# Kernel optimization log

Measured on AMD Instinct MI355X. Metric: run time of the kernel, lower is better.

## Reference

```python
import jax, jax.numpy as jnp
import numpy as np

EMBED_DIM = 512
NUM_HEADS = 8
HEAD_DIM = EMBED_DIM // NUM_HEADS
GRID = 48
BATCH = 8


def _locality_bias(grid_h, grid_w):
    # normalised negative squared L2 distances between patch centres, in [-1, 0]
    gy, gx = jnp.meshgrid(jnp.linspace(0.0, 1.0, grid_h),
                          jnp.linspace(0.0, 1.0, grid_w), indexing='ij')
    coords = jnp.stack([gy.reshape(-1), gx.reshape(-1)], axis=-1)  # (N, 2)
    diff = coords[None, :, :] - coords[:, None, :]                 # (N, N, 2)
    dist2 = jnp.sum(diff * diff, axis=-1)                          # (N, N)
    return -dist2 / jnp.max(dist2)


def setup_inputs() -> dict:
    key = jax.random.key(0)
    k_x, k_qkv, k_pw, k_pb, k_t, k_lw = jax.random.split(key, 6)
    N = GRID * GRID
    x = jax.random.normal(k_x, (BATCH, N, EMBED_DIM), dtype=jnp.float32)
    # torch nn.Linear weights are (out_features, in_features)
    qkv_w = jax.random.normal(k_qkv, (3 * EMBED_DIM, EMBED_DIM), dtype=jnp.float32) * 0.02
    proj_w = jax.random.normal(k_pw, (EMBED_DIM, EMBED_DIM), dtype=jnp.float32) * 0.02
    proj_b = jax.random.normal(k_pb, (EMBED_DIM,), dtype=jnp.float32) * 0.02
    init_temp = float(np.log(HEAD_DIM ** (-0.5)))
    temperature = init_temp + 0.02 * jax.random.normal(k_t, (NUM_HEADS, 1, 1), dtype=jnp.float32)
    locality_weight = 0.1 + 0.02 * jax.random.normal(k_lw, (NUM_HEADS,), dtype=jnp.float32)
    return {
        'x': x,
        'qkv_w': qkv_w,
        'proj_w': proj_w,
        'proj_b': proj_b,
        'temperature': temperature,
        'locality_weight': locality_weight,
        'grid_h': GRID,
        'grid_w': GRID,
    }


def reference(x, qkv_w, proj_w, proj_b, temperature, locality_weight, grid_h, grid_w):
    B, N, C = x.shape
    H = temperature.shape[0]
    D = C // H
    # qkv projection (no bias): (B, N, 3C) -> (3, B, H, N, D)
    qkv = (x @ qkv_w.T).reshape(B, N, 3, H, D)
    qkv = jnp.transpose(qkv, (2, 0, 3, 1, 4))
    q, k, v = qkv[0], qkv[1], qkv[2]              # each (B, H, N, D)
    scale = jnp.exp(temperature)                  # (H, 1, 1) learnable per-head temp
    attn = jnp.einsum('bhqd,bhkd->bhqk', q, k) * scale[None]
    loc = _locality_bias(grid_h, grid_w)          # (N, N), values in [-1, 0]
    attn = attn + locality_weight[None, :, None, None] * loc[None, None]
    attn = jax.nn.softmax(attn, axis=-1)          # dropout is identity (p=0 / eval)
    out = jnp.einsum('bhqk,bhkd->bhqd', attn, v)  # (B, H, N, D)
    out = jnp.transpose(out, (0, 2, 1, 3)).reshape(B, N, C)
    return out @ proj_w.T + proj_b
```

## Files before the change

### kernel.cpp

```cpp
#include <hip/hip_runtime.h>

typedef unsigned int   uint_ma   __attribute__((may_alias));
typedef unsigned short ushort_ma __attribute__((may_alias));
typedef float          float_ma  __attribute__((may_alias));
typedef __bf16 bf16x8 __attribute__((ext_vector_type(8)));
typedef float f32x4 __attribute__((ext_vector_type(4)));
typedef uint_ma u32x4 __attribute__((ext_vector_type(4)));
typedef ushort_ma u16x4 __attribute__((ext_vector_type(4)));

#define BATCH 8
#define NTOK 2304
#define CDIM 512
#define NH 8
#define HD 64
#define MROWS (BATCH * NTOK)
#define LOG2E 1.44269504088896f

constexpr size_t N_X  = (size_t)BATCH * NTOK * CDIM;
constexpr size_t N_WQ = (size_t)3 * CDIM * CDIM;
constexpr size_t N_WP = (size_t)CDIM * CDIM;
constexpr size_t OFF_XO = 0;
constexpr size_t OFF_WQ = OFF_XO + N_X;
constexpr size_t OFF_WP = OFF_WQ + N_WQ;
constexpr size_t OFF_Q  = OFF_WP + N_WP;
constexpr size_t OFF_K  = OFF_Q + N_X;
constexpr size_t OFF_V  = OFF_K + N_X;
constexpr size_t CV8 = (N_X + N_WQ + N_WP) / 8;

__device__ __forceinline__ float bf2f(unsigned short h) {
  unsigned int u = ((unsigned int)h) << 16;
  return __builtin_bit_cast(float, u);
}
__device__ __forceinline__ unsigned short f2bf(float f) {
  unsigned int u = __builtin_bit_cast(unsigned int, f);
  u += 0x7fffu + ((u >> 16) & 1u);
  return (unsigned short)(u >> 16);
}

__device__ __forceinline__ void gload16(const void* g, void* l) {
  __builtin_amdgcn_global_load_lds(
      (const __attribute__((address_space(1))) void*)g,
      (__attribute__((address_space(3))) void*)l, 16, 0, 0);
}

__global__ __launch_bounds__(256) void convert3(
    const float* __restrict__ s0, const float* __restrict__ s1,
    const float* __restrict__ s2, ushort_ma* __restrict__ base) {
  const size_t gid = (size_t)blockIdx.x * blockDim.x + threadIdx.x;
  const size_t stride = (size_t)gridDim.x * blockDim.x;
  for (size_t i = gid; i < CV8; i += stride) {
    size_t r = i;
    const float* src;
    size_t doff;
    if (r < N_X / 8) { src = s0; doff = OFF_XO; }
    else if ((r -= N_X / 8) < N_WQ / 8) { src = s1; doff = OFF_WQ; }
    else { r -= N_WQ / 8; src = s2; doff = OFF_WP; }
    const f32x4* fw = (const f32x4*)(src + r * 8);
    const f32x4 a = fw[0], b = fw[1];
    u16x4 lo, hi;
#pragma unroll
    for (int j = 0; j < 4; j++) { lo[j] = f2bf(a[j]); hi[j] = f2bf(b[j]); }
    ushort_ma* dst = base + doff + r * 8;
    *(u16x4*)dst = lo;
    *(u16x4*)(dst + 4) = hi;
  }
}

template <int MODE>
__global__ __launch_bounds__(256, 3) void gemm_bt(
    const ushort_ma* __restrict__ A, const ushort_ma* __restrict__ W,
    const float* __restrict__ aux,
    unsigned short* __restrict__ o0,
    unsigned short* __restrict__ o1,
    unsigned short* __restrict__ o2)
{
  __shared__ __align__(16) ushort_ma As[2][128][32];
  __shared__ __align__(16) ushort_ma Bs[2][128][32];
  const int K = CDIM;
  const int m0 = blockIdx.x * 128;
  const int n0 = blockIdx.y * 128;
  const int t = threadIdx.x;
  const int lane = t & 63;
  const int w = t >> 6;
  const int wm = (w >> 1) * 64, wn = (w & 1) * 64;
  const int lr = lane & 15, lq = lane >> 4;

  const int srow = w * 16 + (lane >> 2);
  const int scg = (lane & 3) ^ ((srow >> 1) & 3);
  const ushort_ma* Ag0 = A + (size_t)(m0 + srow) * K + scg * 8;
  const ushort_ma* Ag1 = Ag0 + (size_t)64 * K;
  const ushort_ma* Bg0 = W + (size_t)(n0 + srow) * K + scg * 8;
  const ushort_ma* Bg1 = Bg0 + (size_t)64 * K;

  const f32x4 fz = {0.f, 0.f, 0.f, 0.f};
  f32x4 acc[4][4];
#pragma unroll
  for (int i = 0; i < 4; i++)
#pragma unroll
    for (int j = 0; j < 4; j++) acc[i][j] = fz;

  auto issue = [&](int kt, int buf) {
    const int k0 = kt * 32;
    gload16(Ag0 + k0, (void*)&As[buf][w * 16][0]);
    gload16(Ag1 + k0, (void*)&As[buf][64 + w * 16][0]);
    gload16(Bg0 + k0, (void*)&Bs[buf][w * 16][0]);
    gload16(Bg1 + k0, (void*)&Bs[buf][64 + w * 16][0]);
  };

  issue(0, 0);
  const int colf = 8 * (lq ^ ((lr >> 1) & 3));

  for (int kt = 0; kt < 16; kt++) {
    const int buf = kt & 1;
    __syncthreads();
    if (kt < 15) issue(kt + 1, buf ^ 1);
    bf16x8 af[4], bfr[4];
#pragma unroll
    for (int i = 0; i < 4; i++)
      af[i] = __builtin_bit_cast(bf16x8, *(const u32x4*)(&As[buf][wm + i * 16 + lr][colf]));
#pragma unroll
    for (int j = 0; j < 4; j++)
      bfr[j] = __builtin_bit_cast(bf16x8, *(const u32x4*)(&Bs[buf][wn + j * 16 + lr][colf]));
#pragma unroll
    for (int i = 0; i < 4; i++)
#pragma unroll
      for (int j = 0; j < 4; j++)
        acc[i][j] = __builtin_amdgcn_mfma_f32_16x16x32_bf16(af[i], bfr[j], acc[i][j], 0, 0, 0);
  }

  if (MODE == 0) {
#pragma unroll
    for (int j = 0; j < 4; j++) {
      const int gc = n0 + wn + j * 16 + lr;
      const int which = gc >> 9;
      const int h = (gc >> 6) & 7;
      const int d = gc & 63;
#pragma unroll
      for (int i = 0; i < 4; i++) {
        const int gm0 = m0 + wm + i * 16 + lq * 4;
        const int b = gm0 / NTOK;
        const int np = gm0 - b * NTOK;
        if (which == 2) {
          u16x4 pk;
#pragma unroll
          for (int r = 0; r < 4; r++) pk[r] = f2bf(acc[i][j][r]);
          *(u16x4*)(o2 + ((size_t)((b * NH + h) * HD + d)) * NTOK + np) = pk;
        } else {
          const float sc = (which == 0) ? __expf(aux[h]) * LOG2E : 1.0f;
          unsigned short* dst = (which == 0) ? o0 : o1;
          const size_t base = ((size_t)((b * NH + h) * NTOK + np)) * HD + d;
#pragma unroll
          for (int r = 0; r < 4; r++) dst[base + (size_t)r * HD] = f2bf(acc[i][j][r] * sc);
        }
      }
    }
  } else {
    float_ma* outf = (float_ma*)o0;
#pragma unroll
    for (int j = 0; j < 4; j++) {
      const int gc = n0 + wn + j * 16 + lr;
      const float bv = aux[gc];
#pragma unroll
      for (int i = 0; i < 4; i++) {
        const int gm0 = m0 + wm + i * 16 + lq * 4;
#pragma unroll
        for (int r = 0; r < 4; r++)
          outf[(size_t)(gm0 + r) * CDIM + gc] = acc[i][j][r] + bv;
      }
    }
  }
}

__global__ __launch_bounds__(256, 3) void attn_kernel(
    const ushort_ma* __restrict__ Qg,
    const ushort_ma* __restrict__ Kg,
    const ushort_ma* __restrict__ Vg,
    const float* __restrict__ lwp,
    unsigned short* __restrict__ Og)
{
  __shared__ __align__(16) ushort_ma Ks[128][104];
  __shared__ __align__(16) ushort_ma Vs[64][136];
  __shared__ __align__(16) ushort_ma Ps[4][32][32];

  const int bh = blockIdx.y;
  const int b = bh >> 3, h = bh & 7;
  const int q0 = blockIdx.x * 128;
  const int t = threadIdx.x;
  const int lane = t & 63;
  const int w = t >> 6;
  const int lr = lane & 15, lq = lane >> 4;

  if (t < 128) {
    const u32x4 z4 = {0u, 0u, 0u, 0u};
    *(u32x4*)(&Ks[t][72]) = z4;
    *(u32x4*)(&Ks[t][80]) = z4;
    *(u32x4*)(&Ks[t][88]) = z4;
  }
  {
    const ushort_ma* Qb = Qg + ((size_t)bh * NTOK + q0) * HD;
#pragma unroll
    for (int it = 0; it < 4; it++) {
      const int q = t + it * 256;
      const int row = q >> 3, seg = (q & 7) * 8;
      *(u32x4*)(&Ks[row][seg]) = *(const u32x4*)(Qb + (size_t)row * HD + seg);
    }
  }
  __syncthreads();
  bf16x8 aQ[2][2];
#pragma unroll
  for (int mi = 0; mi < 2; mi++)
#pragma unroll
    for (int ks = 0; ks < 2; ks++)
      aQ[mi][ks] = __builtin_bit_cast(
          bf16x8, *(const u32x4*)(&Ks[w * 32 + mi * 16 + lr][ks * 32 + lq * 8]));

  const float cb2 = -0.5f * LOG2E * lwp[h];
  bf16x8 aQb[2];
#pragma unroll
  for (int mi = 0; mi < 2; mi++) {
    const int qrow = q0 + w * 32 + mi * 16 + lr;
    const int yy = qrow / 48;
    const int xx = qrow - yy * 48;
    const float fy = (float)yy * (1.0f / 47.0f);
    const float fx = (float)xx * (1.0f / 47.0f);
    u32x4 v = {0u, 0u, 0u, 0u};
    if (lq == 0) {
      v[0] = (unsigned int)f2bf(fy) | ((unsigned int)f2bf(fx) << 16);
      v[1] = (unsigned int)f2bf(fy * fy + fx * fx) | (0x3F80u << 16);
    }
    aQb[mi] = __builtin_bit_cast(bf16x8, v);
  }

  const u32x4 onesU = {0x3F803F80u, 0x3F803F80u, 0x3F803F80u, 0x3F803F80u};
  const bf16x8 bOnes = __builtin_bit_cast(bf16x8, onesU);

  const f32x4 fz = {0.f, 0.f, 0.f, 0.f};
  f32x4 accO[2][4];
  f32x4 accL[2];
#pragma unroll
  for (int mi = 0; mi < 2; mi++) {
    accL[mi] = fz;
#pragma unroll
    for (int nd = 0; nd < 4; nd++) accO[mi][nd] = fz;
  }

  const ushort_ma* Kb = Kg + (size_t)bh * NTOK * HD;
  const ushort_ma* Vb = Vg + (size_t)bh * HD * NTOK;

  for (int kt = 0; kt < 18; kt++) {
    const int kv0 = kt * 128;
    __syncthreads();
    u32x4 kc[4], vc[4];
#pragma unroll
    for (int it = 0; it < 4; it++) {
      const int q = t + it * 256;
      kc[it] = *(const u32x4*)(Kb + (size_t)(kv0 + (q >> 3)) * HD + (q & 7) * 8);
      vc[it] = *(const u32x4*)(Vb + (size_t)(q >> 4) * NTOK + kv0 + (q & 15) * 8);
    }
#pragma unroll
    for (int it = 0; it < 4; it++) {
      const int q = t + it * 256;
      *(u32x4*)(&Ks[q >> 3][(q & 7) * 8]) = kc[it];
      *(u32x4*)(&Vs[q >> 4][(q & 15) * 8]) = vc[it];
    }
    if (t < 128) {
      const int kv = kv0 + t;
      const int yy = kv / 48;
      const int xx = kv - yy * 48;
      const float fy = (float)yy * (1.0f / 47.0f);
      const float fx = (float)xx * (1.0f / 47.0f);
      u32x4 bv;
      bv[0] = (unsigned int)f2bf(-2.0f * cb2 * fy) |
              ((unsigned int)f2bf(-2.0f * cb2 * fx) << 16);
      bv[1] = (unsigned int)f2bf(cb2) |
              ((unsigned int)f2bf(cb2 * (fy * fy + fx * fx)) << 16);
      bv[2] = 0u;
      bv[3] = 0u;
      *(u32x4*)(&Ks[t][64]) = bv;
    }
    __syncthreads();

#pragma unroll
    for (int c = 0; c < 4; c++) {
      f32x4 s2[2][2] = {{fz, fz}, {fz, fz}};
#pragma unroll
      for (int e2 = 0; e2 < 2; e2++) {
        const int ni = 2 * c + e2;
#pragma unroll
        for (int ks = 0; ks < 3; ks++) {
          const bf16x8 bK = __builtin_bit_cast(
              bf16x8, *(const u32x4*)(&Ks[ni * 16 + lr][ks * 32 + lq * 8]));
#pragma unroll
          for (int mi = 0; mi < 2; mi++) {
            const bf16x8 aOp = (ks < 2) ? aQ[mi][ks] : aQb[mi];
            s2[mi][e2] = __builtin_amdgcn_mfma_f32_16x16x32_bf16(aOp, bK, s2[mi][e2], 0, 0, 0);
          }
        }
      }
#pragma unroll
      for (int e2 = 0; e2 < 2; e2++) {
#pragma unroll
        for (int mi = 0; mi < 2; mi++)
#pragma unroll
          for (int r = 0; r < 4; r++) {
            const float p = __builtin_amdgcn_exp2f(s2[mi][e2][r]);
            const unsigned int pu = __builtin_bit_cast(unsigned int, p);
            const int fw = (2 * lq + (r >> 1)) & 3;
            const int gcol = 8 * ((e2 * 2 + (lr >> 3)) ^ fw) + (lr & 7);
            Ps[w][mi * 16 + lq * 4 + r][gcol] = (unsigned short)(pu >> 16);
          }
      }
      __asm__ volatile("s_waitcnt lgkmcnt(0)" ::: "memory");
      bf16x8 aP[2];
#pragma unroll
      for (int mi = 0; mi < 2; mi++)
        aP[mi] = __builtin_bit_cast(
            bf16x8,
            *(const u32x4*)(&Ps[w][mi * 16 + lr][8 * (lq ^ ((lr >> 1) & 3))]));
#pragma unroll
      for (int nd = 0; nd < 4; nd++) {
        const bf16x8 bV = __builtin_bit_cast(
            bf16x8, *(const u32x4*)(&Vs[nd * 16 + lr][c * 32 + lq * 8]));
#pragma unroll
        for (int mi = 0; mi < 2; mi++)
          accO[mi][nd] = __builtin_amdgcn_mfma_f32_16x16x32_bf16(aP[mi], bV, accO[mi][nd], 0, 0, 0);
      }
#pragma unroll
      for (int mi = 0; mi < 2; mi++)
        accL[mi] = __builtin_amdgcn_mfma_f32_16x16x32_bf16(aP[mi], bOnes, accL[mi], 0, 0, 0);
    }
  }

#pragma unroll
  for (int mi = 0; mi < 2; mi++) {
    f32x4 inv;
#pragma unroll
    for (int r = 0; r < 4; r++) inv[r] = 1.0f / accL[mi][r];
#pragma unroll
    for (int nd = 0; nd < 4; nd++)
#pragma unroll
      for (int r = 0; r < 4; r++) {
        const int np = q0 + w * 32 + mi * 16 + lq * 4 + r;
        Og[((size_t)(b * NTOK + np)) * CDIM + h * HD + nd * 16 + lr] =
            f2bf(accO[mi][nd][r] * inv[r]);
      }
  }
}

extern "C" void kernel_launch(void* const* d_in, const int* in_sizes, int n_in,
                              void* d_out, int out_size, void* d_ws, size_t ws_size,
                              hipStream_t stream) {
  const float* x      = (const float*)d_in[0];
  const float* qkv_w  = (const float*)d_in[1];
  const float* proj_w = (const float*)d_in[2];
  const float* proj_b = (const float*)d_in[3];
  const float* temp   = (const float*)d_in[4];
  const float* lw     = (const float*)d_in[5];

  ushort_ma* base = (ushort_ma*)d_ws;
  ushort_ma* XB  = base + OFF_XO;
  ushort_ma* WQB = base + OFF_WQ;
  ushort_ma* WPB = base + OFF_WP;
  ushort_ma* Q   = base + OFF_Q;
  ushort_ma* Kt  = base + OFF_K;
  ushort_ma* Vt  = base + OFF_V;
  ushort_ma* O   = XB;

  convert3<<<1024, 256, 0, stream>>>(x, qkv_w, proj_w, base);
  gemm_bt<0><<<dim3(MROWS / 128, 1536 / 128), 256, 0, stream>>>(
      XB, WQB, temp, (unsigned short*)Q, (unsigned short*)Kt, (unsigned short*)Vt);
  attn_kernel<<<dim3(NTOK / 128, BATCH * NH), 256, 0, stream>>>(
      Q, Kt, Vt, lw, (unsigned short*)O);
  gemm_bt<1><<<dim3(MROWS / 128, CDIM / 128), 256, 0, stream>>>(
      O, WPB, proj_b, (unsigned short*)d_out, nullptr, nullptr);
}
```

Measured before the change: 300.6 us.

## Enlarge attention query tile to 192 rows and vectorize GEMM epilogue stores

```diff
diff --git a/kernel.cpp b/kernel.cpp
--- a/kernel.cpp
+++ b/kernel.cpp
@@ -125,32 +125,32 @@
     for (int i = 0; i < 4; i++)
 #pragma unroll
       for (int j = 0; j < 4; j++)
-        acc[i][j] = __builtin_amdgcn_mfma_f32_16x16x32_bf16(af[i], bfr[j], acc[i][j], 0, 0, 0);
+        acc[i][j] = __builtin_amdgcn_mfma_f32_16x16x32_bf16(bfr[j], af[i], acc[i][j], 0, 0, 0);
   }
 
   if (MODE == 0) {
 #pragma unroll
     for (int j = 0; j < 4; j++) {
-      const int gc = n0 + wn + j * 16 + lr;
-      const int which = gc >> 9;
-      const int h = (gc >> 6) & 7;
-      const int d = gc & 63;
+      const int gcb = n0 + wn + j * 16 + lq * 4;
+      const int which = gcb >> 9;
+      const int h = (gcb >> 6) & 7;
+      const int db = gcb & 63;
+      const float sc = (which == 0) ? __expf(aux[h]) * LOG2E : 1.0f;
+      unsigned short* dst = (which == 0) ? o0 : o1;
 #pragma unroll
       for (int i = 0; i < 4; i++) {
-        const int gm0 = m0 + wm + i * 16 + lq * 4;
-        const int b = gm0 / NTOK;
-        const int np = gm0 - b * NTOK;
+        const int gm = m0 + wm + i * 16 + lr;
+        const int b = gm / NTOK;
+        const int np = gm - b * NTOK;
         if (which == 2) {
+#pragma unroll
+          for (int r = 0; r < 4; r++)
+            o2[((size_t)((b * NH + h) * HD + db + r)) * NTOK + np] = f2bf(acc[i][j][r]);
+        } else {
           u16x4 pk;
 #pragma unroll
-          for (int r = 0; r < 4; r++) pk[r] = f2bf(acc[i][j][r]);
-          *(u16x4*)(o2 + ((size_t)((b * NH + h) * HD + d)) * NTOK + np) = pk;
-        } else {
-          const float sc = (which == 0) ? __expf(aux[h]) * LOG2E : 1.0f;
-          unsigned short* dst = (which == 0) ? o0 : o1;
-          const size_t base = ((size_t)((b * NH + h) * NTOK + np)) * HD + d;
-#pragma unroll
-          for (int r = 0; r < 4; r++) dst[base + (size_t)r * HD] = f2bf(acc[i][j][r] * sc);
+          for (int r = 0; r < 4; r++) pk[r] = f2bf(acc[i][j][r] * sc);
+          *(u16x4*)(dst + ((size_t)((b * NH + h) * NTOK + np)) * HD + db) = pk;
         }
       }
     }
@@ -158,14 +158,15 @@
     float_ma* outf = (float_ma*)o0;
 #pragma unroll
     for (int j = 0; j < 4; j++) {
-      const int gc = n0 + wn + j * 16 + lr;
-      const float bv = aux[gc];
+      const int gcb = n0 + wn + j * 16 + lq * 4;
+      const f32x4 bv4 = *(const f32x4*)(aux + gcb);
 #pragma unroll
       for (int i = 0; i < 4; i++) {
-        const int gm0 = m0 + wm + i * 16 + lq * 4;
-#pragma unroll
-        for (int r = 0; r < 4; r++)
-          outf[(size_t)(gm0 + r) * CDIM + gc] = acc[i][j][r] + bv;
+        const int gm = m0 + wm + i * 16 + lr;
+        f32x4 ov;
+#pragma unroll
+        for (int r = 0; r < 4; r++) ov[r] = acc[i][j][r] + bv4[r];
+        *(f32x4*)(outf + (size_t)gm * CDIM + gcb) = ov;
       }
     }
   }
@@ -178,47 +179,32 @@
     const float* __restrict__ lwp,
     unsigned short* __restrict__ Og)
 {
-  __shared__ __align__(16) ushort_ma Ks[128][104];
+  __shared__ __align__(16) ushort_ma Ks[128][72];
   __shared__ __align__(16) ushort_ma Vs[64][136];
-  __shared__ __align__(16) ushort_ma Ps[4][32][32];
+  __shared__ __align__(16) ushort_ma Ps[4][48][32];
 
   const int bh = blockIdx.y;
   const int b = bh >> 3, h = bh & 7;
-  const int q0 = blockIdx.x * 128;
+  const int q0 = blockIdx.x * 192;
   const int t = threadIdx.x;
   const int lane = t & 63;
   const int w = t >> 6;
   const int lr = lane & 15, lq = lane >> 4;
 
-  if (t < 128) {
-    const u32x4 z4 = {0u, 0u, 0u, 0u};
-    *(u32x4*)(&Ks[t][72]) = z4;
-    *(u32x4*)(&Ks[t][80]) = z4;
-    *(u32x4*)(&Ks[t][88]) = z4;
-  }
-  {
-    const ushort_ma* Qb = Qg + ((size_t)bh * NTOK + q0) * HD;
-#pragma unroll
-    for (int it = 0; it < 4; it++) {
-      const int q = t + it * 256;
-      const int row = q >> 3, seg = (q & 7) * 8;
-      *(u32x4*)(&Ks[row][seg]) = *(const u32x4*)(Qb + (size_t)row * HD + seg);
-    }
-  }
-  __syncthreads();
-  bf16x8 aQ[2][2];
-#pragma unroll
-  for (int mi = 0; mi < 2; mi++)
+  const ushort_ma* Qw = Qg + ((size_t)bh * NTOK + q0 + (size_t)w * 48) * HD;
+  bf16x8 aQ[3][2];
+#pragma unroll
+  for (int mi = 0; mi < 3; mi++)
 #pragma unroll
     for (int ks = 0; ks < 2; ks++)
       aQ[mi][ks] = __builtin_bit_cast(
-          bf16x8, *(const u32x4*)(&Ks[w * 32 + mi * 16 + lr][ks * 32 + lq * 8]));
+          bf16x8, *(const u32x4*)(Qw + (size_t)(mi * 16 + lr) * HD + ks * 32 + lq * 8));
 
   const float cb2 = -0.5f * LOG2E * lwp[h];
-  bf16x8 aQb[2];
-#pragma unroll
-  for (int mi = 0; mi < 2; mi++) {
-    const int qrow = q0 + w * 32 + mi * 16 + lr;
+  bf16x8 aQb[3];
+#pragma unroll
+  for (int mi = 0; mi < 3; mi++) {
+    const int qrow = q0 + w * 48 + mi * 16 + lr;
     const int yy = qrow / 48;
     const int xx = qrow - yy * 48;
     const float fy = (float)yy * (1.0f / 47.0f);
@@ -235,10 +221,10 @@
   const bf16x8 bOnes = __builtin_bit_cast(bf16x8, onesU);
 
   const f32x4 fz = {0.f, 0.f, 0.f, 0.f};
-  f32x4 accO[2][4];
-  f32x4 accL[2];
-#pragma unroll
-  for (int mi = 0; mi < 2; mi++) {
+  f32x4 accO[3][4];
+  f32x4 accL[3];
+#pragma unroll
+  for (int mi = 0; mi < 3; mi++) {
     accL[mi] = fz;
 #pragma unroll
     for (int nd = 0; nd < 4; nd++) accO[mi][nd] = fz;
@@ -282,25 +268,30 @@
 
 #pragma unroll
     for (int c = 0; c < 4; c++) {
-      f32x4 s2[2][2] = {{fz, fz}, {fz, fz}};
+      f32x4 s2[3][2];
+#pragma unroll
+      for (int mi = 0; mi < 3; mi++) { s2[mi][0] = fz; s2[mi][1] = fz; }
 #pragma unroll
       for (int e2 = 0; e2 < 2; e2++) {
         const int ni = 2 * c + e2;
 #pragma unroll
-        for (int ks = 0; ks < 3; ks++) {
+        for (int ks = 0; ks < 2; ks++) {
           const bf16x8 bK = __builtin_bit_cast(
               bf16x8, *(const u32x4*)(&Ks[ni * 16 + lr][ks * 32 + lq * 8]));
 #pragma unroll
-          for (int mi = 0; mi < 2; mi++) {
-            const bf16x8 aOp = (ks < 2) ? aQ[mi][ks] : aQb[mi];
-            s2[mi][e2] = __builtin_amdgcn_mfma_f32_16x16x32_bf16(aOp, bK, s2[mi][e2], 0, 0, 0);
-          }
+          for (int mi = 0; mi < 3; mi++)
+            s2[mi][e2] = __builtin_amdgcn_mfma_f32_16x16x32_bf16(aQ[mi][ks], bK, s2[mi][e2], 0, 0, 0);
         }
+        const bf16x8 bKb = __builtin_bit_cast(
+            bf16x8, *(const u32x4*)(&Ks[ni * 16 + lr][64]));
+#pragma unroll
+        for (int mi = 0; mi < 3; mi++)
+          s2[mi][e2] = __builtin_amdgcn_mfma_f32_16x16x32_bf16(aQb[mi], bKb, s2[mi][e2], 0, 0, 0);
       }
 #pragma unroll
       for (int e2 = 0; e2 < 2; e2++) {
 #pragma unroll
-        for (int mi = 0; mi < 2; mi++)
+        for (int mi = 0; mi < 3; mi++)
 #pragma unroll
           for (int r = 0; r < 4; r++) {
             const float p = __builtin_amdgcn_exp2f(s2[mi][e2][r]);
@@ -311,9 +302,9 @@
           }
       }
       __asm__ volatile("s_waitcnt lgkmcnt(0)" ::: "memory");
-      bf16x8 aP[2];
-#pragma unroll
-      for (int mi = 0; mi < 2; mi++)
+      bf16x8 aP[3];
+#pragma unroll
+      for (int mi = 0; mi < 3; mi++)
         aP[mi] = __builtin_bit_cast(
             bf16x8,
             *(const u32x4*)(&Ps[w][mi * 16 + lr][8 * (lq ^ ((lr >> 1) & 3))]));
@@ -322,17 +313,17 @@
         const bf16x8 bV = __builtin_bit_cast(
             bf16x8, *(const u32x4*)(&Vs[nd * 16 + lr][c * 32 + lq * 8]));
 #pragma unroll
-        for (int mi = 0; mi < 2; mi++)
+        for (int mi = 0; mi < 3; mi++)
           accO[mi][nd] = __builtin_amdgcn_mfma_f32_16x16x32_bf16(aP[mi], bV, accO[mi][nd], 0, 0, 0);
       }
 #pragma unroll
-      for (int mi = 0; mi < 2; mi++)
+      for (int mi = 0; mi < 3; mi++)
         accL[mi] = __builtin_amdgcn_mfma_f32_16x16x32_bf16(aP[mi], bOnes, accL[mi], 0, 0, 0);
     }
   }
 
 #pragma unroll
-  for (int mi = 0; mi < 2; mi++) {
+  for (int mi = 0; mi < 3; mi++) {
     f32x4 inv;
 #pragma unroll
     for (int r = 0; r < 4; r++) inv[r] = 1.0f / accL[mi][r];
@@ -340,7 +331,7 @@
     for (int nd = 0; nd < 4; nd++)
 #pragma unroll
       for (int r = 0; r < 4; r++) {
-        const int np = q0 + w * 32 + mi * 16 + lq * 4 + r;
+        const int np = q0 + w * 48 + mi * 16 + lq * 4 + r;
         Og[((size_t)(b * NTOK + np)) * CDIM + h * HD + nd * 16 + lr] =
             f2bf(accO[mi][nd][r] * inv[r]);
       }
@@ -369,7 +360,7 @@
   convert3<<<1024, 256, 0, stream>>>(x, qkv_w, proj_w, base);
   gemm_bt<0><<<dim3(MROWS / 128, 1536 / 128), 256, 0, stream>>>(
       XB, WQB, temp, (unsigned short*)Q, (unsigned short*)Kt, (unsigned short*)Vt);
-  attn_kernel<<<dim3(NTOK / 128, BATCH * NH), 256, 0, stream>>>(
+  attn_kernel<<<dim3(NTOK / 192, BATCH * NH), 256, 0, stream>>>(
       Q, Kt, Vt, lw, (unsigned short*)O);
   gemm_bt<1><<<dim3(MROWS / 128, CDIM / 128), 256, 0, stream>>>(
       O, WPB, proj_b, (unsigned short*)d_out, nullptr, nullptr);
```

Measured after the change: 393.6 us. 1.31x slower.
